# Performance work log

Measured on AMD Instinct MI355X. Metric: run time of the kernel, lower is better.

Reference implementation:

```python
import jax, jax.numpy as jnp
import numpy as np

# Llama-2-7B-like GQA attention, prefill over packed equal-length sequences
H = 4096      # hidden_size
NH = 32       # num_attention_heads
NKV = 8       # num_key_value_heads
HD = H // NH  # head_dim = 128
B = 4         # number of packed sequences
S = 1024      # seq_len per sequence
T = B * S     # total packed tokens
BASE = 10000.0  # rope_theta


def setup_inputs() -> dict:
    key = jax.random.key(0)
    ks = jax.random.split(key, 5)
    x = jax.random.normal(ks[0], (T, H), jnp.float32)
    positions = jnp.tile(jnp.arange(S, dtype=jnp.int32), B)  # per-seq positions
    kv_cache = jnp.zeros((1,), jnp.float32)  # placeholder (prefill: kv from current tokens)
    init = 0.02
    wq = jax.random.normal(ks[1], (NH * HD, H), jnp.float32) * init
    wk = jax.random.normal(ks[2], (NKV * HD, H), jnp.float32) * init
    wv = jax.random.normal(ks[3], (NKV * HD, H), jnp.float32) * init
    wo = jax.random.normal(ks[4], (H, NH * HD), jnp.float32) * init
    return {"x": x, "positions": positions, "kv_cache": kv_cache,
            "wq": wq, "wk": wk, "wv": wv, "wo": wo, "seq_len": S}


def _rope(xh, cos_b, sin_b):
    # xh: [T, Hh, D]; cos_b/sin_b: [T, 1, D] (freqs repeat-interleaved by 2)
    half = xh.shape[-1] // 2
    x_rot = jnp.concatenate([-xh[..., half:], xh[..., :half]], axis=-1)
    return xh * cos_b + x_rot * sin_b


def reference(x, positions, kv_cache, wq, wk, wv, wo, seq_len):
    Tn = x.shape[0]
    q = (x @ wq.T).reshape(Tn, NH, HD)
    k = (x @ wk.T).reshape(Tn, NKV, HD)
    v = (x @ wv.T).reshape(Tn, NKV, HD)
    # GQA: repeat_interleave kv heads
    rep = NH // NKV
    k = jnp.repeat(k, rep, axis=1)
    v = jnp.repeat(v, rep, axis=1)
    # RoPE tables (faithful to _precompute_freqs/_rotary_embeddings)
    inv_freq = 1.0 / (BASE ** (jnp.arange(0, HD, 2, dtype=jnp.float32) / HD))
    t = jnp.arange(seq_len, dtype=jnp.float32)
    freqs = t[:, None] * inv_freq[None, :]            # [S, D/2]
    cos, sin = jnp.cos(freqs), jnp.sin(freqs)
    pos = jnp.clip(positions.astype(jnp.int32), 0, seq_len - 1)
    cos_b = jnp.repeat(cos[pos], 2, axis=-1)[:, None, :]  # [T,1,D]
    sin_b = jnp.repeat(sin[pos], 2, axis=-1)[:, None, :]
    q = _rope(q, cos_b, sin_b)
    k = _rope(k, cos_b, sin_b)
    # Paged attention (prefill): causal attention within each packed sequence
    Bn = Tn // seq_len
    qb = q.reshape(Bn, seq_len, NH, HD)
    kb = k.reshape(Bn, seq_len, NH, HD)
    vb = v.reshape(Bn, seq_len, NH, HD)
    scores = jnp.einsum('bqhd,bkhd->bhqk', qb, kb) * (HD ** -0.5)
    causal = jnp.tril(jnp.ones((seq_len, seq_len), bool))
    scores = jnp.where(causal[None, None], scores, -jnp.inf)
    probs = jax.nn.softmax(scores, axis=-1)
    out = jnp.einsum('bhqk,bkhd->bqhd', probs, vb).reshape(Tn, NH * HD)
    return out @ wo.T
```

## Files before the change

kernel.cpp:

```cpp
#include <hip/hip_runtime.h>
#include <hip/hip_bf16.h>
#include <math.h>

#define T_TOK 4096
#define HID   4096
#define NHQ   32
#define NKVH  8
#define HDIM  128
#define SEQ   1024
#define NBATCH 4

typedef __attribute__((ext_vector_type(8))) short bf16x8;
typedef __attribute__((ext_vector_type(4))) float f32x4;

__device__ __forceinline__ unsigned short f2bf(float f) {
  union { float f; unsigned int u; } x; x.f = f;
  unsigned int r = x.u + 0x7FFFu + ((x.u >> 16) & 1u);
  return (unsigned short)(r >> 16);
}

#define GLOAD_LDS16(gp, lp)                                                        \
  __builtin_amdgcn_global_load_lds(                                                \
      (__attribute__((address_space(1))) void*)(unsigned long long)(const void*)(gp), \
      (__attribute__((address_space(3))) void*)(unsigned long long)(const void*)(lp), \
      16, 0, 0)

__global__ __launch_bounds__(256) void cast_all_k(const float* __restrict__ x,
                                                  const float* __restrict__ wq,
                                                  const float* __restrict__ wk,
                                                  const float* __restrict__ wv,
                                                  const float* __restrict__ wo,
                                                  unsigned short* __restrict__ xb,
                                                  unsigned short* __restrict__ wqkv,
                                                  unsigned short* __restrict__ wob) {
  int i = blockIdx.x * 256 + threadIdx.x;
  const float* src; unsigned short* dst; int off;
  if (i < 4194304)       { src = x;  dst = xb;   off = i; }
  else if (i < 8388608)  { src = wq; dst = wqkv; off = i - 4194304; }
  else if (i < 9437184)  { src = wk; dst = wqkv + 16777216; off = i - 8388608; }
  else if (i < 10485760) { src = wv; dst = wqkv + 20971520; off = i - 9437184; }
  else                   { src = wo; dst = wob;  off = i - 10485760; }
  float4 f = ((const float4*)src)[off];
  ushort4 o;
  o.x = f2bf(f.x); o.y = f2bf(f.y); o.z = f2bf(f.z); o.w = f2bf(f.w);
  ((ushort4*)dst)[off] = o;
}

template<bool FUSED>
__global__ __launch_bounds__(512, 1) void gemm256(const unsigned short* __restrict__ A,
                                                  const unsigned short* __restrict__ B,
                                                  float* __restrict__ C,
                                                  const int* __restrict__ pos,
                                                  unsigned short* __restrict__ qr,
                                                  unsigned short* __restrict__ kr,
                                                  unsigned short* __restrict__ vbuf,
                                                  int N) {
  const int K = 4096, nt = 128;
  __shared__ unsigned short AS[4][8192];
  __shared__ unsigned short BS[4][8192];
  const int tid  = threadIdx.x;
  const int lane = tid & 63;
  const int wave = tid >> 6;
  const int m16  = lane & 15;
  const int quad = lane >> 4;
  const int wm   = wave >> 2;
  const int wn   = wave & 3;
  const int hh   = wn >> 1;
  const int bb   = (wn & 1) * 32;

  const int gx = gridDim.x;
  const int nwg = gx * gridDim.y;
  const int orig = blockIdx.y * gx + blockIdx.x;
  const int swz = (orig & 7) * (nwg >> 3) + (orig >> 3);
  const long rowBase = (long)(swz / gx) * 256;
  const long colBase = (long)(swz % gx) * 256;

  const int slot8 = ((quad + 4 * (m16 & 1)) ^ (m16 >> 1)) * 8;
  const int aob = (wm * 64 + (m16 >> 1)) * 64 + slot8;
  const int bob = (hh * 64 + (wn & 1) * 16 + (m16 >> 1)) * 64 + slot8;

  const long Kl = K;
  const int z = (tid & 7) ^ ((tid >> 3) & 7);
  const long srow = 2 * (tid >> 3) + (z >> 2);
  const int sk = (z & 3) * 8;
  const unsigned short* sA = A + (rowBase + srow) * Kl + sk;
  const unsigned short* sB = B + (colBase + srow) * Kl + sk;
  const int dofs = wave * 512;

#define STG_A(sl_, ko_) { GLOAD_LDS16(sA + (ko_),            &AS[sl_][dofs]);         \
                          GLOAD_LDS16(sA + (ko_) + 128 * Kl, &AS[sl_][4096 + dofs]); }
#define STG_B(sl_, ko_) { GLOAD_LDS16(sB + (ko_),            &BS[sl_][dofs]);         \
                          GLOAD_LDS16(sB + (ko_) + 128 * Kl, &BS[sl_][4096 + dofs]); }

#define RD_TILE(sl_) {                                                               \
    _Pragma("unroll")                                                                \
    for (int nf = 0; nf < 4; ++nf)                                                   \
      bfr[nf] = *(const bf16x8*)(&BS[sl_][bob + (nf & 1) * 512 + (nf >> 1) * 2048]); \
    _Pragma("unroll")                                                                \
    for (int mf = 0; mf < 8; ++mf)                                                   \
      af[mf] = *(const bf16x8*)(&AS[sl_][aob + mf * 512]); }

  f32x4 acc[8][4] = {};
  bf16x8 af[8], bfr[4];

  STG_A(0, 0);  STG_B(0, 0);
  STG_A(1, 32); STG_B(1, 32);
  STG_A(2, 64); STG_B(2, 64);
  asm volatile("s_waitcnt vmcnt(4)" ::: "memory");
  __builtin_amdgcn_s_barrier();
  RD_TILE(0);

  for (int g = 0; g < 32; ++g) {
#pragma unroll
    for (int u = 0; u < 4; ++u) {
      const int t = g * 4 + u;
      if (t + 3 < nt) { STG_A((u + 3) & 3, (t + 3) * 32); STG_B((u + 3) & 3, (t + 3) * 32); }
      if (t + 3 < nt) asm volatile("s_waitcnt vmcnt(4)" ::: "memory");
      else            asm volatile("s_waitcnt vmcnt(0)" ::: "memory");
      __builtin_amdgcn_s_setprio(1);
#pragma unroll
      for (int mf = 0; mf < 8; ++mf)
#pragma unroll
        for (int nf = 0; nf < 4; ++nf)
          acc[mf][nf] = __builtin_amdgcn_mfma_f32_16x16x32_bf16(af[mf], bfr[nf], acc[mf][nf], 0, 0, 0);
      __builtin_amdgcn_s_setprio(0);
      if (t + 1 < nt) RD_TILE((u + 1) & 3);
      __builtin_amdgcn_s_barrier();
    }
  }

  if (!FUSED) {
#pragma unroll
    for (int mf = 0; mf < 8; ++mf)
#pragma unroll
      for (int nf = 0; nf < 4; ++nf) {
        long c = colBase + hh * 128 + bb + (nf & 1) * 16 + (nf >> 1) * 64 + m16;
#pragma unroll
        for (int reg = 0; reg < 4; ++reg) {
          long row = rowBase + wm * 128 + mf * 16 + quad * 4 + reg;
          C[row * N + c] = acc[mf][nf][reg];
        }
      }
    return;
  }

  const int n0 = (int)colBase;
  unsigned short* dst;
  int rstride, colofs0;
  bool dorope;
  if (n0 < 4096)       { dst = qr;   rstride = NHQ * HDIM;  colofs0 = n0;        dorope = true; }
  else if (n0 < 5120)  { dst = kr;   rstride = NKVH * HDIM; colofs0 = n0 - 4096; dorope = true; }
  else                 { dst = vbuf; rstride = NKVH * HDIM; colofs0 = n0 - 5120; dorope = false; }
  const int colofs = colofs0 + hh * 128;
  const float c0 = -13.287712379549449f / 64.0f;
  float fA[2], fB[2];
#pragma unroll
  for (int e = 0; e < 2; ++e) {
    int d = bb + e * 16 + m16;
    fA[e] = exp2f(c0 * (float)(d >> 1));
    fB[e] = exp2f(c0 * (float)((d >> 1) + 32));
  }
#pragma unroll
  for (int mf = 0; mf < 8; ++mf) {
#pragma unroll
    for (int reg = 0; reg < 4; ++reg) {
      int grow = (int)rowBase + wm * 128 + mf * 16 + quad * 4 + reg;
      unsigned short* drow = dst + (long)grow * rstride + colofs;
      if (dorope) {
        int p = pos[grow];
        p = p < 0 ? 0 : (p > SEQ - 1 ? SEQ - 1 : p);
        float pf = (float)p;
#pragma unroll
        for (int e = 0; e < 2; ++e) {
          int d = bb + e * 16 + m16;
          float lo = acc[mf][e][reg], hi = acc[mf][e + 2][reg];
          float s1, cc1, s2, cc2;
          __sincosf(pf * fA[e], &s1, &cc1);
          __sincosf(pf * fB[e], &s2, &cc2);
          drow[d]      = f2bf(lo * cc1 - hi * s1);
          drow[d + 64] = f2bf(hi * cc2 + lo * s2);
        }
      } else {
#pragma unroll
        for (int e = 0; e < 2; ++e) {
          int d = bb + e * 16 + m16;
          drow[d]      = f2bf(acc[mf][e][reg]);
          drow[d + 64] = f2bf(acc[mf][e + 2][reg]);
        }
      }
    }
  }
}

#define ATT_SCALE_L2 0.12754227022f
__global__ __launch_bounds__(256) void attn_k(const unsigned short* __restrict__ Qp,
                                              const unsigned short* __restrict__ Kp,
                                              const unsigned short* __restrict__ Vp,
                                              unsigned short* __restrict__ Op) {
  const int pr = blockIdx.x, h = blockIdx.y, b = blockIdx.z;
  const int kvh = h >> 2;
  const int tid = threadIdx.x, wave = tid >> 6, lane = tid & 63;
  const int m16 = lane & 15, quad = lane >> 4;

  __shared__ unsigned short Ks[2][64][128];
  __shared__ unsigned short Vt[128][64];
  __shared__ unsigned short Ps[4][32][64];

  const unsigned short* Kh = Kp + (long)(b * SEQ) * (NKVH * HDIM) + kvh * HDIM;
  const unsigned short* Vh = Vp + (long)(b * SEQ) * (NKVH * HDIM) + kvh * HDIM;

#define STAGE_K(ktv, bufp) {                                               \
    _Pragma("unroll")                                                      \
    for (int it_ = 0; it_ < 4; ++it_) {                                    \
      int c_ = it_ * 256 + tid;                                            \
      int row_ = c_ >> 4, psg_ = c_ & 15;                                  \
      int sg_ = (psg_ & 8) | ((psg_ & 7) ^ (row_ & 7));                    \
      GLOAD_LDS16(Kh + ((long)(ktv) * 64 + row_) * (NKVH * HDIM) + sg_ * 8,\
                  ((unsigned short*)(bufp)) + (it_ * 256 + wave * 64) * 8);\
    } }

#define LOAD_V(ktv, dvv) {                                                 \
    _Pragma("unroll")                                                      \
    for (int it_ = 0; it_ < 4; ++it_)                                      \
      dvv[it_] = *(const uint4*)(Vh + ((long)(ktv) * 64 + lane) * (NKVH * HDIM) + (it_ * 4 + wave) * 8); }

#define SCATTER_V(dvv) {                                                   \
    _Pragma("unroll")                                                      \
    for (int it_ = 0; it_ < 4; ++it_) {                                    \
      const unsigned short* pv_ = (const unsigned short*)&dvv[it_];        \
      int seg_ = it_ * 4 + wave;                                           \
      _Pragma("unroll")                                                    \
      for (int e_ = 0; e_ < 8; ++e_) {                                     \
        int d_ = seg_ * 8 + e_;                                            \
        Vt[d_][((((lane >> 3) + d_) & 7) * 8) + (lane & 7)] = pv_[e_];     \
      } } }

  for (int pass = 0; pass < 2; ++pass) {
    const int qt = pass ? pr : (7 - pr);
    const int qbase = qt * 128;
    const int wq_lo = qbase + wave * 32;

    bf16x8 qa[2][4];
#pragma unroll
    for (int i = 0; i < 2; ++i) {
      const unsigned short* qrow =
          Qp + (long)(b * SEQ + wq_lo + i * 16 + m16) * (NHQ * HDIM) + h * HDIM;
#pragma unroll
      for (int kk = 0; kk < 4; ++kk)
        qa[i][kk] = *(const bf16x8*)(qrow + kk * 32 + quad * 8);
    }

    f32x4 o[2][8] = {};
    float mrow[2][4], lrow[2][4];
#pragma unroll
    for (int i = 0; i < 2; ++i)
#pragma unroll
      for (int r = 0; r < 4; ++r) { mrow[i][r] = -1e30f; lrow[i][r] = 0.f; }

    const int nkt = qt * 2 + 2;

    {
      STAGE_K(0, Ks[0]);
      uint4 dv0[4];
      LOAD_V(0, dv0);
      asm volatile("s_waitcnt vmcnt(0)" ::: "memory");
      SCATTER_V(dv0);
    }
    __syncthreads();

    for (int kt = 0; kt < nkt; ++kt) {
      const int cb = kt & 1;
      const bool active = (kt * 64) <= (wq_lo + 31);
      const bool more = (kt + 1) < nkt;

      f32x4 s4[2][4] = {};
      if (active) {
        __builtin_amdgcn_s_setprio(1);
#pragma unroll
        for (int kk = 0; kk < 4; ++kk) {
          bf16x8 kbf[4];
#pragma unroll
          for (int j = 0; j < 4; ++j) {
            int row = j * 16 + m16;
            int cl = kk * 4 + quad;
            int ps = (cl & 8) | ((cl & 7) ^ (row & 7));
            kbf[j] = *(const bf16x8*)(&Ks[cb][row][ps * 8]);
          }
#pragma unroll
          for (int i = 0; i < 2; ++i)
#pragma unroll
            for (int j = 0; j < 4; ++j)
              s4[i][j] = __builtin_amdgcn_mfma_f32_16x16x32_bf16(qa[i][kk], kbf[j], s4[i][j], 0, 0, 0);
        }
        __builtin_amdgcn_s_setprio(0);
      }

      uint4 dv[4];
      if (more) {
        STAGE_K(kt + 1, Ks[cb ^ 1]);
        LOAD_V(kt + 1, dv);
      }
      asm volatile("" ::: "memory");

      if (active) {
        const bool full = (kt * 64 + 63) <= wq_lo;
#pragma unroll
        for (int i = 0; i < 2; ++i) {
#pragma unroll
          for (int r = 0; r < 4; ++r) {
            const int qrow = i * 16 + quad * 4 + r;
            const int qi = qbase + wave * 32 + qrow;
            float v[4];
#pragma unroll
            for (int j = 0; j < 4; ++j) {
              v[j] = s4[i][j][r] * ATT_SCALE_L2;
              if (!full && (kt * 64 + j * 16 + m16 > qi)) v[j] = -1e30f;
            }
            float mx = fmaxf(fmaxf(v[0], v[1]), fmaxf(v[2], v[3]));
            mx = fmaxf(mx, __shfl_xor(mx, 1));
            mx = fmaxf(mx, __shfl_xor(mx, 2));
            mx = fmaxf(mx, __shfl_xor(mx, 4));
            mx = fmaxf(mx, __shfl_xor(mx, 8));
            float mold = mrow[i][r];
            float mnew = fmaxf(mold, mx);
            float alpha = exp2f(mold - mnew);
            float rs = 0.f;
#pragma unroll
            for (int j = 0; j < 4; ++j) {
              float pj = exp2f(v[j] - mnew);
              rs += pj;
              int col = j * 16 + m16;
              Ps[wave][qrow][((((col >> 3) + qrow) & 7) * 8) + (col & 7)] = f2bf(pj);
            }
            rs += __shfl_xor(rs, 1); rs += __shfl_xor(rs, 2);
            rs += __shfl_xor(rs, 4); rs += __shfl_xor(rs, 8);
            lrow[i][r] = lrow[i][r] * alpha + rs;
            mrow[i][r] = mnew;
#pragma unroll
            for (int n = 0; n < 8; ++n) o[i][n][r] *= alpha;
          }
        }
        __builtin_amdgcn_s_setprio(1);
#pragma unroll
        for (int kk = 0; kk < 2; ++kk) {
          bf16x8 pa[2], vb[8];
#pragma unroll
          for (int i = 0; i < 2; ++i) {
            int row = i * 16 + m16;
            pa[i] = *(const bf16x8*)(&Ps[wave][row][(((kk * 4 + quad) + row) & 7) * 8]);
          }
#pragma unroll
          for (int n = 0; n < 8; ++n) {
            int row = n * 16 + m16;
            vb[n] = *(const bf16x8*)(&Vt[row][(((kk * 4 + quad) + row) & 7) * 8]);
          }
#pragma unroll
          for (int i = 0; i < 2; ++i)
#pragma unroll
            for (int n = 0; n < 8; ++n)
              o[i][n] = __builtin_amdgcn_mfma_f32_16x16x32_bf16(pa[i], vb[n], o[i][n], 0, 0, 0);
        }
        __builtin_amdgcn_s_setprio(0);
      }

      __syncthreads();
      if (more) SCATTER_V(dv);
      __syncthreads();
    }

#pragma unroll
    for (int i = 0; i < 2; ++i) {
#pragma unroll
      for (int r = 0; r < 4; ++r) {
        float inv = 1.0f / lrow[i][r];
        unsigned short* orow =
            Op + (long)(b * SEQ + wq_lo + i * 16 + quad * 4 + r) * (NHQ * HDIM) + h * HDIM;
#pragma unroll
        for (int n = 0; n < 8; ++n)
          orow[n * 16 + m16] = f2bf(o[i][n][r] * inv);
      }
    }
  }
}

extern "C" void kernel_launch(void* const* d_in, const int* in_sizes, int n_in,
                              void* d_out, int out_size, void* d_ws, size_t ws_size,
                              hipStream_t stream) {
  (void)in_sizes; (void)n_in; (void)out_size; (void)ws_size;
  const float* x  = (const float*)d_in[0];
  const int* pos  = (const int*)d_in[1];
  const float* wq = (const float*)d_in[3];
  const float* wk = (const float*)d_in[4];
  const float* wv = (const float*)d_in[5];
  const float* wo = (const float*)d_in[6];
  float* out = (float*)d_out;

  char* ws = (char*)d_ws;
  unsigned short* xb    = (unsigned short*)(ws);
  unsigned short* wqkv  = (unsigned short*)(ws + (32ll << 20));
  unsigned short* wob   = (unsigned short*)(ws + (80ll << 20));
  unsigned short* qr    = (unsigned short*)(ws + (112ll << 20));
  unsigned short* kr    = (unsigned short*)(ws + (144ll << 20));
  unsigned short* vb_   = (unsigned short*)(ws + (152ll << 20));
  unsigned short* ao    = (unsigned short*)(ws + (160ll << 20));

  cast_all_k<<<57344, 256, 0, stream>>>(x, wq, wk, wv, wo, xb, wqkv, wob);
  gemm256<true><<<dim3(24, 16), 512, 0, stream>>>(xb, wqkv, nullptr, pos, qr, kr, vb_, 6144);
  attn_k<<<dim3(4, 32, 4), 256, 0, stream>>>(qr, kr, vb_, ao);
  gemm256<false><<<dim3(16, 16), 512, 0, stream>>>(ao, wob, out, nullptr, nullptr, nullptr, nullptr, 4096);
}
```

Before: 754.6 us.

## Restructure GEMM mainloop into 8-phase ping-pong schedule with K=64 double-buffered tiles

Replaces the 4-stage K=32 GEMM pipeline with a double-buffered K=64 scheme. Each 256x256 tile is split into four 128x128 quadrants, and MFMA work on one quadrant is interleaved with LDS reads and global-to-LDS staging of the next, separated by barriers. The goal is to hide LDS and global latency better and halve the number of main-loop iterations. The cost is many more barriers per step and different register pressure for both the QKV and output projection GEMMs.

```diff
diff --git a/kernel.cpp b/kernel.cpp
--- a/kernel.cpp
+++ b/kernel.cpp
@@ -47,26 +47,24 @@
 }
 
 template<bool FUSED>
-__global__ __launch_bounds__(512, 1) void gemm256(const unsigned short* __restrict__ A,
-                                                  const unsigned short* __restrict__ B,
-                                                  float* __restrict__ C,
-                                                  const int* __restrict__ pos,
-                                                  unsigned short* __restrict__ qr,
-                                                  unsigned short* __restrict__ kr,
-                                                  unsigned short* __restrict__ vbuf,
-                                                  int N) {
-  const int K = 4096, nt = 128;
-  __shared__ unsigned short AS[4][8192];
-  __shared__ unsigned short BS[4][8192];
+__global__ __launch_bounds__(512, 1) void gemm8p(const unsigned short* __restrict__ A,
+                                                 const unsigned short* __restrict__ B,
+                                                 float* __restrict__ C,
+                                                 const int* __restrict__ pos,
+                                                 unsigned short* __restrict__ qr,
+                                                 unsigned short* __restrict__ kr,
+                                                 unsigned short* __restrict__ vbuf,
+                                                 int N) {
+  const int K = 4096, nt = 64;
+  __shared__ unsigned short AS[2][2][128][64];
+  __shared__ unsigned short BS[2][2][128][64];
   const int tid  = threadIdx.x;
   const int lane = tid & 63;
   const int wave = tid >> 6;
   const int m16  = lane & 15;
   const int quad = lane >> 4;
-  const int wm   = wave >> 2;
-  const int wn   = wave & 3;
-  const int hh   = wn >> 1;
-  const int bb   = (wn & 1) * 32;
+  const int wm2  = wave >> 2;
+  const int wn2  = wave & 3;
 
   const int gx = gridDim.x;
   const int nwg = gx * gridDim.y;
@@ -75,121 +73,146 @@
   const long rowBase = (long)(swz / gx) * 256;
   const long colBase = (long)(swz % gx) * 256;
 
-  const int slot8 = ((quad + 4 * (m16 & 1)) ^ (m16 >> 1)) * 8;
-  const int aob = (wm * 64 + (m16 >> 1)) * 64 + slot8;
-  const int bob = (hh * 64 + (wn & 1) * 16 + (m16 >> 1)) * 64 + slot8;
+  int aof[2], bof[2];
+#pragma unroll
+  for (int ks = 0; ks < 2; ++ks) {
+    int sx = ((ks * 4 + quad) ^ (m16 & 7)) * 8;
+    aof[ks] = (wm2 * 64 + m16) * 64 + sx;
+    bof[ks] = (wn2 * 16 + m16) * 64 + sx;
+  }
 
   const long Kl = K;
-  const int z = (tid & 7) ^ ((tid >> 3) & 7);
-  const long srow = 2 * (tid >> 3) + (z >> 2);
-  const int sk = (z & 3) * 8;
-  const unsigned short* sA = A + (rowBase + srow) * Kl + sk;
-  const unsigned short* sB = B + (colBase + srow) * Kl + sk;
+  const int sck = ((tid & 7) ^ ((tid >> 3) & 7)) * 8;
+  const unsigned short* gA = A + (rowBase + (tid >> 3)) * Kl + sck;
+  const unsigned short* gB = B + (colBase + (tid >> 3)) * Kl + sck;
   const int dofs = wave * 512;
 
-#define STG_A(sl_, ko_) { GLOAD_LDS16(sA + (ko_),            &AS[sl_][dofs]);         \
-                          GLOAD_LDS16(sA + (ko_) + 128 * Kl, &AS[sl_][4096 + dofs]); }
-#define STG_B(sl_, ko_) { GLOAD_LDS16(sB + (ko_),            &BS[sl_][dofs]);         \
-                          GLOAD_LDS16(sB + (ko_) + 128 * Kl, &BS[sl_][4096 + dofs]); }
-
-#define RD_TILE(sl_) {                                                               \
-    _Pragma("unroll")                                                                \
-    for (int nf = 0; nf < 4; ++nf)                                                   \
-      bfr[nf] = *(const bf16x8*)(&BS[sl_][bob + (nf & 1) * 512 + (nf >> 1) * 2048]); \
-    _Pragma("unroll")                                                                \
-    for (int mf = 0; mf < 8; ++mf)                                                   \
-      af[mf] = *(const bf16x8*)(&AS[sl_][aob + mf * 512]); }
-
-  f32x4 acc[8][4] = {};
-  bf16x8 af[8], bfr[4];
-
-  STG_A(0, 0);  STG_B(0, 0);
-  STG_A(1, 32); STG_B(1, 32);
-  STG_A(2, 64); STG_B(2, 64);
-  asm volatile("s_waitcnt vmcnt(4)" ::: "memory");
+#define STG(XS_, gX_, db_, hf_, ko_) {                                                      \
+    GLOAD_LDS16(gX_ + (long)((hf_) * 128) * Kl + (ko_),      ((unsigned short*)&XS_[db_][hf_][0][0]) + dofs);  \
+    GLOAD_LDS16(gX_ + (long)((hf_) * 128 + 64) * Kl + (ko_), ((unsigned short*)&XS_[db_][hf_][64][0]) + dofs); }
+
+#define RD_A(d_, qa_) {                                                   \
+    const unsigned short* Ah_ = &AS[d_][qa_][0][0];                       \
+    _Pragma("unroll") for (int mf = 0; mf < 4; ++mf)                      \
+      _Pragma("unroll") for (int ks = 0; ks < 2; ++ks)                    \
+        af[mf][ks] = *(const bf16x8*)(Ah_ + aof[ks] + mf * 1024); }
+
+#define RD_B(d_, qb_, dst_) {                                             \
+    const unsigned short* Bh_ = &BS[d_][qb_][0][0];                       \
+    _Pragma("unroll") for (int nf = 0; nf < 2; ++nf)                      \
+      _Pragma("unroll") for (int ks = 0; ks < 2; ++ks)                    \
+        dst_[nf][ks] = *(const bf16x8*)(Bh_ + bof[ks] + nf * 4096); }
+
+#define MFMA16(qa_, qb_, b_) {                                            \
+    _Pragma("unroll") for (int mf = 0; mf < 4; ++mf)                      \
+      _Pragma("unroll") for (int nf = 0; nf < 2; ++nf)                    \
+        _Pragma("unroll") for (int ks = 0; ks < 2; ++ks)                  \
+          acc[qa_][qb_][mf][nf] = __builtin_amdgcn_mfma_f32_16x16x32_bf16(\
+              af[mf][ks], b_[nf][ks], acc[qa_][qb_][mf][nf], 0, 0, 0); }
+
+  f32x4 acc[2][2][4][2] = {};
+  bf16x8 af[4][2], b0[2][2], b1[2][2];
+
+  STG(AS, gA, 0, 0, 0);   STG(BS, gB, 0, 1, 0);
+  STG(AS, gA, 0, 1, 0);   STG(BS, gB, 0, 0, 0);
+  STG(AS, gA, 1, 0, 64);  STG(BS, gB, 1, 1, 64);
+  STG(AS, gA, 1, 1, 64);
+  asm volatile("s_waitcnt vmcnt(6)" ::: "memory");
   __builtin_amdgcn_s_barrier();
-  RD_TILE(0);
-
-  for (int g = 0; g < 32; ++g) {
-#pragma unroll
-    for (int u = 0; u < 4; ++u) {
-      const int t = g * 4 + u;
-      if (t + 3 < nt) { STG_A((u + 3) & 3, (t + 3) * 32); STG_B((u + 3) & 3, (t + 3) * 32); }
-      if (t + 3 < nt) asm volatile("s_waitcnt vmcnt(4)" ::: "memory");
-      else            asm volatile("s_waitcnt vmcnt(0)" ::: "memory");
-      __builtin_amdgcn_s_setprio(1);
-#pragma unroll
-      for (int mf = 0; mf < 8; ++mf)
-#pragma unroll
-        for (int nf = 0; nf < 4; ++nf)
-          acc[mf][nf] = __builtin_amdgcn_mfma_f32_16x16x32_bf16(af[mf], bfr[nf], acc[mf][nf], 0, 0, 0);
-      __builtin_amdgcn_s_setprio(0);
-      if (t + 1 < nt) RD_TILE((u + 1) & 3);
-      __builtin_amdgcn_s_barrier();
-    }
+
+#define KSTEP(n_, d_) {                                                               \
+                                \
+    RD_A(d_, 0); RD_B(d_, 0, b0);                                                     \
+    if ((n_) + 1 < nt) STG(BS, gB, (d_) ^ 1, 0, ((n_) + 1) * 64);                     \
+    asm volatile("s_waitcnt lgkmcnt(8)" ::: "memory");                                \
+    __builtin_amdgcn_s_barrier();                                                     \
+    asm volatile("s_waitcnt lgkmcnt(0)" ::: "memory");                                \
+    __builtin_amdgcn_s_setprio(1); MFMA16(0, 0, b0); __builtin_amdgcn_s_setprio(0);   \
+    __builtin_amdgcn_s_barrier();                                                     \
+                                 \
+    RD_B(d_, 1, b1);                                                                  \
+    if ((n_) + 2 < nt) STG(AS, gA, d_, 0, ((n_) + 2) * 64);                           \
+    __builtin_amdgcn_s_barrier();                                                     \
+    asm volatile("s_waitcnt lgkmcnt(0)" ::: "memory");                                \
+    __builtin_amdgcn_s_setprio(1); MFMA16(0, 1, b1); __builtin_amdgcn_s_setprio(0);   \
+    __builtin_amdgcn_s_barrier();                                                     \
+                                 \
+    RD_A(d_, 1);                                                                      \
+    if ((n_) + 2 < nt) STG(BS, gB, d_, 1, ((n_) + 2) * 64);                           \
+    __builtin_amdgcn_s_barrier();                                                     \
+    asm volatile("s_waitcnt lgkmcnt(0)" ::: "memory");                                \
+    __builtin_amdgcn_s_setprio(1); MFMA16(1, 1, b1); __builtin_amdgcn_s_setprio(0);   \
+    __builtin_amdgcn_s_barrier();                                                     \
+                  \
+    if ((n_) + 2 < nt) STG(AS, gA, d_, 1, ((n_) + 2) * 64);                           \
+    __builtin_amdgcn_s_barrier();                                                     \
+    __builtin_amdgcn_s_setprio(1); MFMA16(1, 0, b0); __builtin_amdgcn_s_setprio(0);   \
+    if ((n_) + 2 < nt) asm volatile("s_waitcnt vmcnt(6)" ::: "memory");               \
+    else               asm volatile("s_waitcnt vmcnt(0)" ::: "memory");               \
+    __builtin_amdgcn_s_barrier(); }
+
+  for (int it = 0; it < 32; ++it) {
+    KSTEP(2 * it, 0);
+    KSTEP(2 * it + 1, 1);
   }
 
   if (!FUSED) {
 #pragma unroll
-    for (int mf = 0; mf < 8; ++mf)
-#pragma unroll
-      for (int nf = 0; nf < 4; ++nf) {
-        long c = colBase + hh * 128 + bb + (nf & 1) * 16 + (nf >> 1) * 64 + m16;
-#pragma unroll
-        for (int reg = 0; reg < 4; ++reg) {
-          long row = rowBase + wm * 128 + mf * 16 + quad * 4 + reg;
-          C[row * N + c] = acc[mf][nf][reg];
+    for (int qa = 0; qa < 2; ++qa)
+#pragma unroll
+      for (int qb = 0; qb < 2; ++qb)
+#pragma unroll
+        for (int mf = 0; mf < 4; ++mf)
+#pragma unroll
+          for (int nf = 0; nf < 2; ++nf) {
+            long c = colBase + qb * 128 + wn2 * 16 + nf * 64 + m16;
+#pragma unroll
+            for (int reg = 0; reg < 4; ++reg) {
+              long row = rowBase + qa * 128 + wm2 * 64 + mf * 16 + quad * 4 + reg;
+              C[row * N + c] = acc[qa][qb][mf][nf][reg];
+            }
+          }
+    return;
+  }
+
+  const int n0 = (int)colBase;
+  unsigned short* dst; long rstride; int colofs; bool dorope;
+  if (n0 < 4096)       { dst = qr;   rstride = NHQ * HDIM;  colofs = n0;        dorope = true; }
+  else if (n0 < 5120)  { dst = kr;   rstride = NKVH * HDIM; colofs = n0 - 4096; dorope = true; }
+  else                 { dst = vbuf; rstride = NKVH * HDIM; colofs = n0 - 5120; dorope = false; }
+  const float c0v = -13.287712379549449f / 64.0f;
+  const int dD = wn2 * 16 + m16;
+  const float f1 = exp2f(c0v * (float)(dD >> 1));
+  const float f2 = exp2f(c0v * (float)((dD >> 1) + 32));
+#pragma unroll
+  for (int qa = 0; qa < 2; ++qa)
+#pragma unroll
+    for (int mf = 0; mf < 4; ++mf)
+#pragma unroll
+      for (int reg = 0; reg < 4; ++reg) {
+        int grow = (int)rowBase + qa * 128 + wm2 * 64 + mf * 16 + quad * 4 + reg;
+        unsigned short* drow = dst + (long)grow * rstride + colofs;
+        if (dorope) {
+          int p = pos[grow];
+          p = p < 0 ? 0 : (p > SEQ - 1 ? SEQ - 1 : p);
+          float pf = (float)p;
+          float s1, c1, s2, c2;
+          __sincosf(pf * f1, &s1, &c1);
+          __sincosf(pf * f2, &s2, &c2);
+#pragma unroll
+          for (int qb = 0; qb < 2; ++qb) {
+            float lo = acc[qa][qb][mf][0][reg], hi = acc[qa][qb][mf][1][reg];
+            drow[qb * 128 + dD]      = f2bf(lo * c1 - hi * s1);
+            drow[qb * 128 + dD + 64] = f2bf(hi * c2 + lo * s2);
+          }
+        } else {
+#pragma unroll
+          for (int qb = 0; qb < 2; ++qb) {
+            drow[qb * 128 + dD]      = f2bf(acc[qa][qb][mf][0][reg]);
+            drow[qb * 128 + dD + 64] = f2bf(acc[qa][qb][mf][1][reg]);
+          }
         }
       }
-    return;
-  }
-
-  const int n0 = (int)colBase;
-  unsigned short* dst;
-  int rstride, colofs0;
-  bool dorope;
-  if (n0 < 4096)       { dst = qr;   rstride = NHQ * HDIM;  colofs0 = n0;        dorope = true; }
-  else if (n0 < 5120)  { dst = kr;   rstride = NKVH * HDIM; colofs0 = n0 - 4096; dorope = true; }
-  else                 { dst = vbuf; rstride = NKVH * HDIM; colofs0 = n0 - 5120; dorope = false; }
-  const int colofs = colofs0 + hh * 128;
-  const float c0 = -13.287712379549449f / 64.0f;
-  float fA[2], fB[2];
-#pragma unroll
-  for (int e = 0; e < 2; ++e) {
-    int d = bb + e * 16 + m16;
-    fA[e] = exp2f(c0 * (float)(d >> 1));
-    fB[e] = exp2f(c0 * (float)((d >> 1) + 32));
-  }
-#pragma unroll
-  for (int mf = 0; mf < 8; ++mf) {
-#pragma unroll
-    for (int reg = 0; reg < 4; ++reg) {
-      int grow = (int)rowBase + wm * 128 + mf * 16 + quad * 4 + reg;
-      unsigned short* drow = dst + (long)grow * rstride + colofs;
-      if (dorope) {
-        int p = pos[grow];
-        p = p < 0 ? 0 : (p > SEQ - 1 ? SEQ - 1 : p);
-        float pf = (float)p;
-#pragma unroll
-        for (int e = 0; e < 2; ++e) {
-          int d = bb + e * 16 + m16;
-          float lo = acc[mf][e][reg], hi = acc[mf][e + 2][reg];
-          float s1, cc1, s2, cc2;
-          __sincosf(pf * fA[e], &s1, &cc1);
-          __sincosf(pf * fB[e], &s2, &cc2);
-          drow[d]      = f2bf(lo * cc1 - hi * s1);
-          drow[d + 64] = f2bf(hi * cc2 + lo * s2);
-        }
-      } else {
-#pragma unroll
-        for (int e = 0; e < 2; ++e) {
-          int d = bb + e * 16 + m16;
-          drow[d]      = f2bf(acc[mf][e][reg]);
-          drow[d + 64] = f2bf(acc[mf][e + 2][reg]);
-        }
-      }
-    }
-  }
 }
 
 #define ATT_SCALE_L2 0.12754227022f
@@ -405,7 +428,7 @@
   unsigned short* ao    = (unsigned short*)(ws + (160ll << 20));
 
   cast_all_k<<<57344, 256, 0, stream>>>(x, wq, wk, wv, wo, xb, wqkv, wob);
-  gemm256<true><<<dim3(24, 16), 512, 0, stream>>>(xb, wqkv, nullptr, pos, qr, kr, vb_, 6144);
+  gemm8p<true><<<dim3(24, 16), 512, 0, stream>>>(xb, wqkv, nullptr, pos, qr, kr, vb_, 6144);
   attn_k<<<dim3(4, 32, 4), 256, 0, stream>>>(qr, kr, vb_, ao);
-  gemm256<false><<<dim3(16, 16), 512, 0, stream>>>(ao, wob, out, nullptr, nullptr, nullptr, nullptr, 4096);
+  gemm8p<false><<<dim3(16, 16), 512, 0, stream>>>(ao, wob, out, nullptr, nullptr, nullptr, nullptr, 4096);
 }
```

Result: no change. 744.4 us (-1.4%).
